# Optimization experiments

Measured on AMD Instinct MI355X. Metric: run time of the kernel, lower is better.

## Reference

```python
import jax, jax.numpy as jnp
import numpy as np
import math

V = 32000; SMAX = 256; N = 512; M = 16; TICKS = 4; D = 512
NSA = 256; NSO = 512; H = 8; HD = D // H; B = 2; S = 256


def _ln(x, g, b, eps=1e-5):
    m = x.mean(-1, keepdims=True)
    v = ((x - m) ** 2).mean(-1, keepdims=True)
    return (x - m) / jnp.sqrt(v + eps) * g + b


def _glu(x):
    a, b = jnp.split(x, 2, axis=-1)
    return a * jax.nn.sigmoid(b)


def setup_inputs() -> dict:
    key = jax.random.key(0)
    ks = iter(jax.random.split(key, 64))
    rn = lambda shape, s: jax.random.normal(next(ks), shape, jnp.float32) * s
    inp = {}
    inp['x'] = jax.random.randint(next(ks), (B, S), 0, V)
    inp['tok_table'] = rn((V, D), 0.02)
    inp['pos_embed'] = rn((SMAX, D), 0.02)
    inp['ln_emb_g'] = jnp.ones(D); inp['ln_emb_b'] = jnp.zeros(D)
    inp['kv_w'] = rn((D, D), 1 / math.sqrt(D)); inp['kv_b'] = jnp.zeros(D)
    inp['kv_ln_g'] = jnp.ones(D); inp['kv_ln_b'] = jnp.zeros(D)
    inp['q_w'] = rn((NSA, D), 1 / math.sqrt(NSA)); inp['q_b'] = jnp.zeros(D)
    inp['wq'] = rn((D, D), 1 / math.sqrt(D)); inp['bq'] = jnp.zeros(D)
    inp['wk'] = rn((D, D), 1 / math.sqrt(D)); inp['bk'] = jnp.zeros(D)
    inp['wv'] = rn((D, D), 1 / math.sqrt(D)); inp['bv'] = jnp.zeros(D)
    inp['ow'] = rn((D, D), 1 / math.sqrt(D)); inp['ob'] = jnp.zeros(D)
    inp['syn_w'] = rn((D + N, 2 * N), 1 / math.sqrt(D + N)); inp['syn_b'] = jnp.zeros(2 * N)
    inp['syn_g'] = jnp.ones(N); inp['syn_beta'] = jnp.zeros(N)
    inp['fc1_w'] = rn((N, M, 256), math.sqrt(2.0 / M)); inp['fc1_b'] = jnp.zeros((N, 256))
    inp['fc2_w'] = rn((N, 128, 2), math.sqrt(2.0 / 128)); inp['fc2_b'] = jnp.zeros((N, 2))
    inp['nlm_T'] = jnp.ones(1)
    a = math.sqrt(1.0 / N)
    inp['start_act'] = jax.random.uniform(next(ks), (SMAX, N), jnp.float32, -a, a)
    b2 = math.sqrt(1.0 / (N + M))
    inp['start_trace'] = jax.random.uniform(next(ks), (SMAX, N, M), jnp.float32, -b2, b2)
    inp['decay_a'] = jnp.zeros(NSA); inp['decay_o'] = jnp.zeros(NSO)
    inp['out_w'] = rn((NSO, V), 1 / math.sqrt(NSO)); inp['out_b'] = jnp.zeros(V)
    inp['idx_al'] = jax.random.randint(next(ks), (NSA,), 0, N)
    inp['idx_ar'] = jax.random.randint(next(ks), (NSA,), 0, N)
    inp['idx_ol'] = jax.random.randint(next(ks), (NSO,), 0, N)
    inp['idx_or'] = jax.random.randint(next(ks), (NSO,), 0, N)
    return inp


def reference(x, tok_table, pos_embed, ln_emb_g, ln_emb_b, kv_w, kv_b, kv_ln_g, kv_ln_b,
              q_w, q_b, wq, bq, wk, bk, wv, bv, ow, ob, syn_w, syn_b, syn_g, syn_beta,
              fc1_w, fc1_b, fc2_w, fc2_b, nlm_T, start_act, start_trace, decay_a, decay_o,
              out_w, out_b, idx_al, idx_ar, idx_ol, idx_or):
    Bz, Sl = x.shape
    emb = _ln(tok_table[x] + pos_embed[:Sl], ln_emb_g, ln_emb_b)        # (B,S,D)
    kv = _ln(emb @ kv_w + kv_b, kv_ln_g, kv_ln_b)
    k = (kv @ wk + bk).reshape(Bz, Sl, H, HD)                            # keys/values fixed over ticks
    v = (kv @ wv + bv).reshape(Bz, Sl, H, HD)
    mask = jnp.triu(jnp.ones((Sl, Sl), bool), 1)                         # True = masked
    r_a = jnp.exp(-decay_a)
    r_o = jnp.exp(-decay_o)
    act = jnp.broadcast_to(start_act[:Sl], (Bz, Sl, N))
    trace = jnp.broadcast_to(start_trace[:Sl], (Bz, Sl, N, M))
    aa = ba = ao_ = bo = None
    preds, certs = [], []
    for _ in range(TICKS):
        # action synchronization (decayed pairwise product)
        pp = act[:, :, idx_al] * act[:, :, idx_ar]
        if aa is None:
            aa, ba = pp, jnp.ones_like(pp)
        else:
            aa, ba = r_a * aa + pp, r_a * ba + 1.0
        sync_a = aa / jnp.sqrt(ba + 1e-8)
        # causal attention with query from action sync
        qh = ((sync_a @ q_w + q_b) @ wq + bq).reshape(Bz, Sl, H, HD)
        sc = jnp.einsum('bqhd,bkhd->bhqk', qh, k) / math.sqrt(HD)
        sc = jnp.where(mask, -1e9, sc)
        attn_out = jnp.einsum('bhqk,bkhd->bqhd', jax.nn.softmax(sc, -1), v).reshape(Bz, Sl, D) @ ow + ob
        # synapse MLP -> new pre-activation, shift memory trace
        state = _ln(_glu(jnp.concatenate([attn_out, act], -1) @ syn_w + syn_b), syn_g, syn_beta)
        trace = jnp.concatenate([trace[..., 1:], state[..., None]], -1)
        # per-neuron NLM (batched private GEMMs)
        h = _glu(jnp.einsum('bsnm,nmh->bsnh', trace, fc1_w) + fc1_b)
        o = _glu(jnp.einsum('bsnh,nho->bsno', h, fc2_w) + fc2_b)
        act = o[..., 0] / nlm_T[0]
        # output synchronization + prediction
        ppo = act[:, :, idx_ol] * act[:, :, idx_or]
        if ao_ is None:
            ao_, bo = ppo, jnp.ones_like(ppo)
        else:
            ao_, bo = r_o * ao_ + ppo, r_o * bo + 1.0
        pred = (ao_ / jnp.sqrt(bo + 1e-8)) @ out_w + out_b                # (B,S,V)
        p = jax.nn.softmax(pred, -1)
        ent = -(p * jnp.log(p + 1e-10)).sum(-1) / math.log(V)
        preds.append(pred)
        certs.append(jnp.stack([ent, 1.0 - ent], -1))
    return jnp.stack(preds, -1), jnp.stack(certs, -1)
```

## Files before the change

### kernel.cpp

```cpp
#include <hip/hip_runtime.h>
#include <cstdint>
#include <cstddef>

#define BATCH 2
#define SEQ   256
#define DIM   512
#define NN    512
#define MM    16
#define NTICK 4
#define NSA   256
#define NSO   512
#define NHEAD 8
#define HDIM  64
#define VOCAB 32000
#define BS    (BATCH*SEQ)

typedef __bf16 bf16;
typedef bf16  bf16x4  __attribute__((ext_vector_type(4)));
typedef bf16  bf16x8v __attribute__((ext_vector_type(8)));
typedef float f32x4   __attribute__((ext_vector_type(4)));

__global__ __launch_bounds__(128) void embed_kernel(const int* __restrict__ x,
    const float* __restrict__ tok, const float* __restrict__ pos, float* __restrict__ out){
  int row = blockIdx.x;
  int s = row & (SEQ-1);
  int token = x[row];
  const float4* tr = (const float4*)(tok + (size_t)token*DIM);
  const float4* pr = (const float4*)(pos + (size_t)s*DIM);
  float4* orow = (float4*)(out + (size_t)row*DIM);
  for (int i = threadIdx.x; i < DIM/4; i += blockDim.x){
    float4 a = tr[i], b = pr[i];
    float4 o; o.x=a.x+b.x; o.y=a.y+b.y; o.z=a.z+b.z; o.w=a.w+b.w;
    orow[i] = o;
  }
}

__global__ __launch_bounds__(256) void ln512_kernel(const float* __restrict__ in,
    const float* __restrict__ g, const float* __restrict__ b, float* __restrict__ out){
  int row = blockIdx.x, tid = threadIdx.x;
  const float* xr = in + (size_t)row*512;
  float v0 = xr[tid], v1 = xr[tid+256];
  float s = v0+v1, ss = v0*v0+v1*v1;
  #pragma unroll
  for (int o = 32; o > 0; o >>= 1){ s += __shfl_down(s, o); ss += __shfl_down(ss, o); }
  __shared__ float rs[4], rss[4];
  __shared__ float smean, sinv;
  int wid = tid >> 6, lane = tid & 63;
  if (lane == 0){ rs[wid] = s; rss[wid] = ss; }
  __syncthreads();
  if (tid == 0){
    float S = rs[0]+rs[1]+rs[2]+rs[3];
    float SS = rss[0]+rss[1]+rss[2]+rss[3];
    float m = S * (1.0f/512.0f);
    float var = SS * (1.0f/512.0f) - m*m;
    smean = m; sinv = 1.0f/sqrtf(var + 1e-5f);
  }
  __syncthreads();
  float m = smean, inv = sinv;
  out[(size_t)row*512 + tid]       = (v0-m)*inv*g[tid]     + b[tid];
  out[(size_t)row*512 + tid + 256] = (v1-m)*inv*g[tid+256] + b[tid+256];
}

__global__ __launch_bounds__(256) void glu_ln_kernel(const float* __restrict__ y,
    const float* __restrict__ g, const float* __restrict__ beta, float* __restrict__ out){
  int row = blockIdx.x, tid = threadIdx.x;
  const float* yr = y + (size_t)row*1024;
  float a0 = yr[tid],     b0 = yr[tid+512];
  float a1 = yr[tid+256], b1 = yr[tid+768];
  float g0 = a0 / (1.0f + expf(-b0));
  float g1 = a1 / (1.0f + expf(-b1));
  float s = g0+g1, ss = g0*g0+g1*g1;
  #pragma unroll
  for (int o = 32; o > 0; o >>= 1){ s += __shfl_down(s, o); ss += __shfl_down(ss, o); }
  __shared__ float rs[4], rss[4];
  __shared__ float smean, sinv;
  int wid = tid >> 6, lane = tid & 63;
  if (lane == 0){ rs[wid] = s; rss[wid] = ss; }
  __syncthreads();
  if (tid == 0){
    float S = rs[0]+rs[1]+rs[2]+rs[3];
    float SS = rss[0]+rss[1]+rss[2]+rss[3];
    float m = S * (1.0f/512.0f);
    float var = SS * (1.0f/512.0f) - m*m;
    smean = m; sinv = 1.0f/sqrtf(var + 1e-5f);
  }
  __syncthreads();
  float m = smean, inv = sinv;
  out[(size_t)row*512 + tid]       = (g0-m)*inv*g[tid]     + beta[tid];
  out[(size_t)row*512 + tid + 256] = (g1-m)*inv*g[tid+256] + beta[tid+256];
}

__global__ __launch_bounds__(256) void sync_kernel(const float* __restrict__ act,
    const int* __restrict__ il, const int* __restrict__ ir, const float* __restrict__ decay,
    float* __restrict__ accA, float* __restrict__ accB,
    float* __restrict__ outf, bf16* __restrict__ outb, int NS, int first){
  int i = blockIdx.x*256 + threadIdx.x;
  if (i >= BS*NS) return;
  int bs = i / NS, c = i - bs*NS;
  const float* ar = act + (size_t)bs*NN;
  float p = ar[il[c]] * ar[ir[c]];
  float A, Bv;
  if (first){ A = p; Bv = 1.0f; }
  else {
    float r = expf(-decay[c]);
    A = r*accA[i] + p;
    Bv = r*accB[i] + 1.0f;
  }
  accA[i] = A; accB[i] = Bv;
  float sy = A / sqrtf(Bv + 1e-8f);
  if (outf) outf[i] = sy;
  if (outb) outb[i] = (bf16)sy;
}

__global__ __launch_bounds__(128) void gemm_f32(
    const float* __restrict__ A, const float* __restrict__ W,
    const float* __restrict__ bias, float* __restrict__ C,
    int Mr, int Nc, int Kd, int lda, int ldc){
  __shared__ float As[16][36];
  __shared__ float Ws[16][64];
  int tid = threadIdx.x;
  int tx = tid & 15, ty = tid >> 4;
  int bm = blockIdx.y * 32, bn = blockIdx.x * 64;
  float acc[4][4] = {};
  int lm = tid >> 2, lkq = tid & 3;
  int wn4 = tid & 15, wkr = tid >> 4;
  for (int k0 = 0; k0 < Kd; k0 += 16){
    float4 a4 = *(const float4*)(A + (size_t)(bm+lm)*lda + k0 + lkq*4);
    float4 w0 = *(const float4*)(W + (size_t)(k0+wkr)*Nc + bn + wn4*4);
    float4 w1 = *(const float4*)(W + (size_t)(k0+wkr+8)*Nc + bn + wn4*4);
    As[lkq*4+0][lm] = a4.x; As[lkq*4+1][lm] = a4.y;
    As[lkq*4+2][lm] = a4.z; As[lkq*4+3][lm] = a4.w;
    *(float4*)&Ws[wkr][wn4*4]   = w0;
    *(float4*)&Ws[wkr+8][wn4*4] = w1;
    __syncthreads();
    #pragma unroll
    for (int kk = 0; kk < 16; kk++){
      float4 av = *(const float4*)&As[kk][ty*4];
      float4 wv = *(const float4*)&Ws[kk][tx*4];
      float ar[4] = {av.x, av.y, av.z, av.w};
      float wr[4] = {wv.x, wv.y, wv.z, wv.w};
      #pragma unroll
      for (int i = 0; i < 4; i++)
        #pragma unroll
        for (int j = 0; j < 4; j++)
          acc[i][j] = fmaf(ar[i], wr[j], acc[i][j]);
    }
    __syncthreads();
  }
  float4 b4 = {0,0,0,0};
  if (bias) b4 = *(const float4*)(bias + bn + tx*4);
  #pragma unroll
  for (int i = 0; i < 4; i++){
    int row = bm + ty*4 + i;
    float4 o;
    o.x = acc[i][0]+b4.x; o.y = acc[i][1]+b4.y;
    o.z = acc[i][2]+b4.z; o.w = acc[i][3]+b4.w;
    *(float4*)(C + (size_t)row*ldc + bn + tx*4) = o;
  }
}

__global__ void qbc_kernel(const float* __restrict__ qb, const float* __restrict__ wq,
                           const float* __restrict__ bq, float* __restrict__ qbc){
  int j = blockIdx.x*64 + threadIdx.x;
  float s = bq[j];
  for (int k = 0; k < DIM; k++) s = fmaf(qb[k], wq[(size_t)k*DIM + j], s);
  qbc[j] = s;
}

__global__ __launch_bounds__(256) void attn_kernel(const float* __restrict__ qh,
    const float* __restrict__ kb, const float* __restrict__ vb, float* __restrict__ outb){
  int qt = blockIdx.x, h = blockIdx.y, b = blockIdx.z;
  __shared__ float qs[16][HDIM];
  __shared__ float sc[16][SEQ + 4];
  __shared__ float red[16][16];
  __shared__ float rowm[16], rowz[16];
  int tid = threadIdx.x;
  {
    int r = tid >> 4, c4 = tid & 15;
    *(float4*)&qs[r][c4*4] =
      *(const float4*)(qh + ((size_t)(b*SEQ + qt*16 + r))*DIM + h*HDIM + c4*4);
  }
  __syncthreads();
  {
    int kk = tid;
    const float* krow = kb + ((size_t)(b*SEQ + kk))*DIM + h*HDIM;
    float s[16] = {};
    for (int d4 = 0; d4 < HDIM/4; d4++){
      float4 k4 = *(const float4*)(krow + d4*4);
      #pragma unroll
      for (int q = 0; q < 16; q++){
        float4 q4 = *(const float4*)&qs[q][d4*4];
        s[q] += q4.x*k4.x + q4.y*k4.y + q4.z*k4.z + q4.w*k4.w;
      }
    }
    #pragma unroll
    for (int q = 0; q < 16; q++){
      int qg = qt*16 + q;
      sc[q][kk] = (kk > qg) ? -1e9f : s[q]*0.125f;
    }
  }
  __syncthreads();
  {
    int q = tid >> 4, seg = tid & 15;
    float m = -1e30f;
    for (int i = 0; i < 16; i++) m = fmaxf(m, sc[q][seg*16+i]);
    red[q][seg] = m;
  }
  __syncthreads();
  if (tid < 16){
    float m = red[tid][0];
    for (int i = 1; i < 16; i++) m = fmaxf(m, red[tid][i]);
    rowm[tid] = m;
  }
  __syncthreads();
  {
    int q = tid >> 4, seg = tid & 15;
    float m = rowm[q], z = 0.0f;
    for (int i = 0; i < 16; i++){
      float e = expf(sc[q][seg*16+i] - m);
      sc[q][seg*16+i] = e;
      z += e;
    }
    red[q][seg] = z;
  }
  __syncthreads();
  if (tid < 16){
    float z = 0.0f;
    for (int i = 0; i < 16; i++) z += red[tid][i];
    rowz[tid] = 1.0f / z;
  }
  __syncthreads();
  {
    int q = tid >> 4, dc = tid & 15;
    float inv = rowz[q];
    float ax=0, ay=0, az=0, aw=0;
    for (int kk = 0; kk < SEQ; kk++){
      float p = sc[q][kk];
      float4 v4 = *(const float4*)(vb + ((size_t)(b*SEQ + kk))*DIM + h*HDIM + dc*4);
      ax = fmaf(p, v4.x, ax); ay = fmaf(p, v4.y, ay);
      az = fmaf(p, v4.z, az); aw = fmaf(p, v4.w, aw);
    }
    float4 o; o.x=ax*inv; o.y=ay*inv; o.z=az*inv; o.w=aw*inv;
    *(float4*)(outb + ((size_t)(b*SEQ + qt*16 + q))*DIM + h*HDIM + dc*4) = o;
  }
}

__global__ void act_init_kernel(const float* __restrict__ sa, float* __restrict__ act){
  int i = blockIdx.x*256 + threadIdx.x;
  act[i] = sa[i & (SEQ*NN - 1)];
}
__global__ void cat_act_kernel(const float* __restrict__ act, float* __restrict__ cat){
  int i = blockIdx.x*256 + threadIdx.x;
  int bs = i >> 9, n = i & 511;
  cat[(size_t)bs*1024 + 512 + n] = act[i];
}

__global__ __launch_bounds__(256) void nlm_kernel(
    const float* __restrict__ start_trace,
    const float* __restrict__ s0, const float* __restrict__ s1,
    const float* __restrict__ s2, const float* __restrict__ s3,
    const float* __restrict__ fc1w, const float* __restrict__ fc1b,
    const float* __restrict__ fc2w, const float* __restrict__ fc2b,
    const float* __restrict__ nlmT, float* __restrict__ act, int t){
  int n = blockIdx.x, b = blockIdx.y, s = threadIdx.x;
  int bs = b*SEQ + s;
  size_t sidx = (size_t)bs*NN + n;
  float tr[16];
  #pragma unroll
  for (int j = 0; j < 16; j++){
    int src = j + t + 1;
    if (src < 16){
      tr[j] = start_trace[((size_t)s*NN + n)*MM + src];
    } else {
      int k = src - 16;
      tr[j] = (k==0) ? s0[sidx] : (k==1) ? s1[sidx] : (k==2) ? s2[sidx] : s3[sidx];
    }
  }
  const float* w1 = fc1w + (size_t)n*16*256;
  const float* b1 = fc1b + (size_t)n*256;
  const float* w2 = fc2w + (size_t)n*256;
  float o0 = fc2b[n*2+0], o1 = fc2b[n*2+1];
  #pragma unroll 4
  for (int j = 0; j < 128; j++){
    float a  = b1[j];
    float bb = b1[j+128];
    #pragma unroll
    for (int m = 0; m < 16; m++){
      a  = fmaf(tr[m], w1[m*256 + j],       a);
      bb = fmaf(tr[m], w1[m*256 + j + 128], bb);
    }
    float gg = a / (1.0f + expf(-bb));
    o0 = fmaf(gg, w2[j*2+0], o0);
    o1 = fmaf(gg, w2[j*2+1], o1);
  }
  float o = o0 / (1.0f + expf(-o1));
  act[sidx] = o / nlmT[0];
}

__global__ __launch_bounds__(256) void out_gemm(
    const bf16* __restrict__ sy0, const bf16* __restrict__ sy1,
    const bf16* __restrict__ sy2, const bf16* __restrict__ sy3,
    const float* __restrict__ Wo, const float* __restrict__ bo,
    float* __restrict__ outp){
  __shared__ bf16 BsT[128][40];
  int tid = threadIdx.x;
  int m0 = blockIdx.x * 64;
  int n0 = blockIdx.y * 128;
  int wid = tid >> 6, lane = tid & 63;
  int ln = lane & 15, kq = lane >> 4;
  int mrow = m0 + wid*16 + ln;
  const bf16* sy[4] = {sy0, sy1, sy2, sy3};
  f32x4 acc[4][8];
  #pragma unroll
  for (int t = 0; t < 4; t++)
    #pragma unroll
    for (int nt = 0; nt < 8; nt++) acc[t][nt] = (f32x4){0.f,0.f,0.f,0.f};
  int snq = tid & 31, sk2 = tid >> 5;
  for (int k0 = 0; k0 < 512; k0 += 32){
    {
      const float* src = Wo + (size_t)(k0 + sk2*4)*VOCAB + n0 + snq*4;
      float4 r0 = *(const float4*)(src);
      float4 r1 = *(const float4*)(src + VOCAB);
      float4 r2 = *(const float4*)(src + 2*(size_t)VOCAB);
      float4 r3 = *(const float4*)(src + 3*(size_t)VOCAB);
      float c0[4] = {r0.x,r0.y,r0.z,r0.w};
      float c1[4] = {r1.x,r1.y,r1.z,r1.w};
      float c2[4] = {r2.x,r2.y,r2.z,r2.w};
      float c3[4] = {r3.x,r3.y,r3.z,r3.w};
      #pragma unroll
      for (int i = 0; i < 4; i++){
        bf16x4 pk;
        pk[0]=(bf16)c0[i]; pk[1]=(bf16)c1[i]; pk[2]=(bf16)c2[i]; pk[3]=(bf16)c3[i];
        *(bf16x4*)&BsT[snq*4+i][sk2*4] = pk;
      }
    }
    __syncthreads();
    bf16x8v af[4];
    #pragma unroll
    for (int t = 0; t < 4; t++)
      af[t] = *(const bf16x8v*)(sy[t] + (size_t)mrow*512 + k0 + kq*8);
    #pragma unroll
    for (int nt = 0; nt < 8; nt++){
      bf16x8v bfr = *(const bf16x8v*)&BsT[nt*16 + ln][kq*8];
      #pragma unroll
      for (int t = 0; t < 4; t++)
        acc[t][nt] = __builtin_amdgcn_mfma_f32_16x16x32_bf16(af[t], bfr, acc[t][nt], 0, 0, 0);
    }
    __syncthreads();
  }
  #pragma unroll
  for (int nt = 0; nt < 8; nt++){
    int col = n0 + nt*16 + ln;
    float bb = bo[col];
    #pragma unroll
    for (int r = 0; r < 4; r++){
      int row = m0 + wid*16 + kq*4 + r;
      float4 o;
      o.x = acc[0][nt][r] + bb;
      o.y = acc[1][nt][r] + bb;
      o.z = acc[2][nt][r] + bb;
      o.w = acc[3][nt][r] + bb;
      *(float4*)(outp + ((size_t)row*VOCAB + col)*4) = o;
    }
  }
}

__global__ __launch_bounds__(256) void entropy_kernel(
    const float* __restrict__ preds, float* __restrict__ certs){
  int bs = blockIdx.x, tid = threadIdx.x;
  const float4* row = (const float4*)(preds + (size_t)bs*VOCAB*4);
  float m0=-1e30f, m1=-1e30f, m2=-1e30f, m3=-1e30f;
  for (int v = tid; v < VOCAB; v += 256){
    float4 x = row[v];
    m0 = fmaxf(m0, x.x); m1 = fmaxf(m1, x.y);
    m2 = fmaxf(m2, x.z); m3 = fmaxf(m3, x.w);
  }
  #pragma unroll
  for (int o = 32; o > 0; o >>= 1){
    m0 = fmaxf(m0, __shfl_down(m0, o)); m1 = fmaxf(m1, __shfl_down(m1, o));
    m2 = fmaxf(m2, __shfl_down(m2, o)); m3 = fmaxf(m3, __shfl_down(m3, o));
  }
  __shared__ float rm[4][4];
  __shared__ float fm[4];
  int wid = tid >> 6, lane = tid & 63;
  if (lane == 0){ rm[wid][0]=m0; rm[wid][1]=m1; rm[wid][2]=m2; rm[wid][3]=m3; }
  __syncthreads();
  if (tid == 0){
    #pragma unroll
    for (int t = 0; t < 4; t++)
      fm[t] = fmaxf(fmaxf(rm[0][t], rm[1][t]), fmaxf(rm[2][t], rm[3][t]));
  }
  __syncthreads();
  m0=fm[0]; m1=fm[1]; m2=fm[2]; m3=fm[3];
  float z0=0,z1=0,z2=0,z3=0, s0=0,s1=0,s2=0,s3=0;
  for (int v = tid; v < VOCAB; v += 256){
    float4 x = row[v];
    float e;
    e = expf(x.x-m0); z0 += e; s0 = fmaf(e, x.x-m0, s0);
    e = expf(x.y-m1); z1 += e; s1 = fmaf(e, x.y-m1, s1);
    e = expf(x.z-m2); z2 += e; s2 = fmaf(e, x.z-m2, s2);
    e = expf(x.w-m3); z3 += e; s3 = fmaf(e, x.w-m3, s3);
  }
  #pragma unroll
  for (int o = 32; o > 0; o >>= 1){
    z0 += __shfl_down(z0,o); z1 += __shfl_down(z1,o);
    z2 += __shfl_down(z2,o); z3 += __shfl_down(z3,o);
    s0 += __shfl_down(s0,o); s1 += __shfl_down(s1,o);
    s2 += __shfl_down(s2,o); s3 += __shfl_down(s3,o);
  }
  __shared__ float rz[4][8];
  if (lane == 0){
    rz[wid][0]=z0; rz[wid][1]=z1; rz[wid][2]=z2; rz[wid][3]=z3;
    rz[wid][4]=s0; rz[wid][5]=s1; rz[wid][6]=s2; rz[wid][7]=s3;
  }
  __syncthreads();
  if (tid == 0){
    float inv_logV = 1.0f / logf((float)VOCAB);
    #pragma unroll
    for (int t = 0; t < 4; t++){
      float Z = rz[0][t]+rz[1][t]+rz[2][t]+rz[3][t];
      float Ss = rz[0][t+4]+rz[1][t+4]+rz[2][t+4]+rz[3][t+4];
      float ent = (logf(Z) - Ss/Z) * inv_logV;
      certs[((size_t)bs*2 + 0)*4 + t] = ent;
      certs[((size_t)bs*2 + 1)*4 + t] = 1.0f - ent;
    }
  }
}

extern "C" void kernel_launch(void* const* d_in, const int* in_sizes, int n_in,
                              void* d_out, int out_size, void* d_ws, size_t ws_size,
                              hipStream_t stream){
  const int*   x        = (const int*)  d_in[0];
  const float* tok      = (const float*)d_in[1];
  const float* pos      = (const float*)d_in[2];
  const float* ln_emb_g = (const float*)d_in[3];
  const float* ln_emb_b = (const float*)d_in[4];
  const float* kv_w     = (const float*)d_in[5];
  const float* kv_b     = (const float*)d_in[6];
  const float* kv_ln_g  = (const float*)d_in[7];
  const float* kv_ln_b  = (const float*)d_in[8];
  const float* q_w      = (const float*)d_in[9];
  const float* q_b      = (const float*)d_in[10];
  const float* wq       = (const float*)d_in[11];
  const float* bq       = (const float*)d_in[12];
  const float* wk       = (const float*)d_in[13];
  const float* bk       = (const float*)d_in[14];
  const float* wv       = (const float*)d_in[15];
  const float* bv       = (const float*)d_in[16];
  const float* ow       = (const float*)d_in[17];
  const float* ob       = (const float*)d_in[18];
  const float* syn_w    = (const float*)d_in[19];
  const float* syn_b    = (const float*)d_in[20];
  const float* syn_g    = (const float*)d_in[21];
  const float* syn_beta = (const float*)d_in[22];
  const float* fc1_w    = (const float*)d_in[23];
  const float* fc1_b    = (const float*)d_in[24];
  const float* fc2_w    = (const float*)d_in[25];
  const float* fc2_b    = (const float*)d_in[26];
  const float* nlm_T    = (const float*)d_in[27];
  const float* start_act   = (const float*)d_in[28];
  const float* start_trace = (const float*)d_in[29];
  const float* decay_a  = (const float*)d_in[30];
  const float* decay_o  = (const float*)d_in[31];
  const float* out_w    = (const float*)d_in[32];
  const float* out_b    = (const float*)d_in[33];
  const int* idx_al = (const int*)d_in[34];
  const int* idx_ar = (const int*)d_in[35];
  const int* idx_ol = (const int*)d_in[36];
  const int* idx_or = (const int*)d_in[37];

  char* wp = (char*)d_ws;
  auto alloc = [&](size_t bytes) -> void* {
    void* p = (void*)wp;
    wp += (bytes + 255) & ~(size_t)255;
    return p;
  };
  float* qwc      = (float*)alloc((size_t)256*512*4);
  float* qbc      = (float*)alloc(512*4);
  float* emb_raw  = (float*)alloc((size_t)BS*512*4);
  float* emb      = (float*)alloc((size_t)BS*512*4);
  float* kvt      = (float*)alloc((size_t)BS*512*4);
  float* kvn      = (float*)alloc((size_t)BS*512*4);
  float* kbuf     = (float*)alloc((size_t)BS*512*4);
  float* vbuf     = (float*)alloc((size_t)BS*512*4);
  float* act      = (float*)alloc((size_t)BS*512*4);
  float* aaB      = (float*)alloc((size_t)BS*256*4);
  float* baB      = (float*)alloc((size_t)BS*256*4);
  float* aoB      = (float*)alloc((size_t)BS*512*4);
  float* boB      = (float*)alloc((size_t)BS*512*4);
  float* sync_a   = (float*)alloc((size_t)BS*256*4);
  float* qh       = (float*)alloc((size_t)BS*512*4);
  float* attn_raw = (float*)alloc((size_t)BS*512*4);
  float* catb     = (float*)alloc((size_t)BS*1024*4);
  float* syn_y    = (float*)alloc((size_t)BS*1024*4);
  float* states[NTICK];
  for (int t = 0; t < NTICK; t++) states[t] = (float*)alloc((size_t)BS*512*4);
  bf16* syob[NTICK];
  for (int t = 0; t < NTICK; t++) syob[t] = (bf16*)alloc((size_t)BS*512*2);

  float* preds = (float*)d_out;
  float* certs = (float*)d_out + (size_t)BS*VOCAB*NTICK;

  embed_kernel<<<BS, 128, 0, stream>>>(x, tok, pos, emb_raw);
  ln512_kernel<<<BS, 256, 0, stream>>>(emb_raw, ln_emb_g, ln_emb_b, emb);
  gemm_f32<<<dim3(512/64, 512/32), 128, 0, stream>>>(emb, kv_w, kv_b, kvt, 512,512,512, 512,512);
  ln512_kernel<<<BS, 256, 0, stream>>>(kvt, kv_ln_g, kv_ln_b, kvn);
  gemm_f32<<<dim3(512/64, 512/32), 128, 0, stream>>>(kvn, wk, bk, kbuf, 512,512,512, 512,512);
  gemm_f32<<<dim3(512/64, 512/32), 128, 0, stream>>>(kvn, wv, bv, vbuf, 512,512,512, 512,512);
  gemm_f32<<<dim3(512/64, 256/32), 128, 0, stream>>>(q_w, wq, nullptr, qwc, 256,512,512, 512,512);
  qbc_kernel<<<8, 64, 0, stream>>>(q_b, wq, bq, qbc);
  act_init_kernel<<<(BS*NN)/256, 256, 0, stream>>>(start_act, act);

  for (int t = 0; t < NTICK; t++){
    sync_kernel<<<(BS*NSA)/256, 256, 0, stream>>>(act, idx_al, idx_ar, decay_a,
        aaB, baB, sync_a, nullptr, NSA, t==0);
    gemm_f32<<<dim3(512/64, 512/32), 128, 0, stream>>>(sync_a, qwc, qbc, qh, 512,512,256, 256,512);
    attn_kernel<<<dim3(16, NHEAD, BATCH), 256, 0, stream>>>(qh, kbuf, vbuf, attn_raw);
    gemm_f32<<<dim3(512/64, 512/32), 128, 0, stream>>>(attn_raw, ow, ob, catb, 512,512,512, 512,1024);
    cat_act_kernel<<<(BS*NN)/256, 256, 0, stream>>>(act, catb);
    gemm_f32<<<dim3(1024/64, 512/32), 128, 0, stream>>>(catb, syn_w, syn_b, syn_y, 512,1024,1024, 1024,1024);
    glu_ln_kernel<<<BS, 256, 0, stream>>>(syn_y, syn_g, syn_beta, states[t]);
    nlm_kernel<<<dim3(NN, BATCH), 256, 0, stream>>>(start_trace,
        states[0], states[1], states[2], states[3],
        fc1_w, fc1_b, fc2_w, fc2_b, nlm_T, act, t);
    sync_kernel<<<(BS*NSO)/256, 256, 0, stream>>>(act, idx_ol, idx_or, decay_o,
        aoB, boB, nullptr, syob[t], NSO, t==0);
  }

  out_gemm<<<dim3(BS/64, VOCAB/128), 256, 0, stream>>>(
      syob[0], syob[1], syob[2], syob[3], out_w, out_b, preds);
  entropy_kernel<<<BS, 256, 0, stream>>>(preds, certs);
}
```

Before: 1.643 ms.

## Use split-bf16 MFMA GEMMs, pre-transposed bf16 weights, and fuse entropy into output GEMM

Replaces the scalar fp32 GEMM with an MFMA kernel that emulates fp32 precision using three bf16 products (hi*hi, lo*hi, hi*lo) on pre-split, transposed weights. The output projection now reads a pre-transposed bf16 copy of out_w directly, without staging through shared memory. It also computes per-block softmax max, sum and entropy partials in its epilogue, and a small kernel merges them, so the separate full pass over the logits is gone. In exchange, extra weight split/transpose kernels run on every call, and precision drops slightly.

```diff
diff --git a/kernel.cpp b/kernel.cpp
--- a/kernel.cpp
+++ b/kernel.cpp
@@ -14,6 +14,7 @@
 #define HDIM  64
 #define VOCAB 32000
 #define BS    (BATCH*SEQ)
+#define NBLK  250
 
 typedef __bf16 bf16;
 typedef bf16  bf16x4  __attribute__((ext_vector_type(4)));
@@ -112,50 +113,68 @@
   if (outb) outb[i] = (bf16)sy;
 }
 
-__global__ __launch_bounds__(128) void gemm_f32(
-    const float* __restrict__ A, const float* __restrict__ W,
-    const float* __restrict__ bias, float* __restrict__ C,
-    int Mr, int Nc, int Kd, int lda, int ldc){
-  __shared__ float As[16][36];
-  __shared__ float Ws[16][64];
+__global__ __launch_bounds__(256) void split_t(const float* __restrict__ W,
+    bf16* __restrict__ hiT, bf16* __restrict__ loT, int K, int N){
+  __shared__ float t[32][33];
+  int n0 = blockIdx.x*32, k0 = blockIdx.y*32;
   int tid = threadIdx.x;
-  int tx = tid & 15, ty = tid >> 4;
-  int bm = blockIdx.y * 32, bn = blockIdx.x * 64;
-  float acc[4][4] = {};
-  int lm = tid >> 2, lkq = tid & 3;
-  int wn4 = tid & 15, wkr = tid >> 4;
-  for (int k0 = 0; k0 < Kd; k0 += 16){
-    float4 a4 = *(const float4*)(A + (size_t)(bm+lm)*lda + k0 + lkq*4);
-    float4 w0 = *(const float4*)(W + (size_t)(k0+wkr)*Nc + bn + wn4*4);
-    float4 w1 = *(const float4*)(W + (size_t)(k0+wkr+8)*Nc + bn + wn4*4);
-    As[lkq*4+0][lm] = a4.x; As[lkq*4+1][lm] = a4.y;
-    As[lkq*4+2][lm] = a4.z; As[lkq*4+3][lm] = a4.w;
-    *(float4*)&Ws[wkr][wn4*4]   = w0;
-    *(float4*)&Ws[wkr+8][wn4*4] = w1;
-    __syncthreads();
-    #pragma unroll
-    for (int kk = 0; kk < 16; kk++){
-      float4 av = *(const float4*)&As[kk][ty*4];
-      float4 wv = *(const float4*)&Ws[kk][tx*4];
-      float ar[4] = {av.x, av.y, av.z, av.w};
-      float wr[4] = {wv.x, wv.y, wv.z, wv.w};
-      #pragma unroll
-      for (int i = 0; i < 4; i++)
-        #pragma unroll
-        for (int j = 0; j < 4; j++)
-          acc[i][j] = fmaf(ar[i], wr[j], acc[i][j]);
-    }
-    __syncthreads();
-  }
-  float4 b4 = {0,0,0,0};
-  if (bias) b4 = *(const float4*)(bias + bn + tx*4);
-  #pragma unroll
-  for (int i = 0; i < 4; i++){
-    int row = bm + ty*4 + i;
-    float4 o;
-    o.x = acc[i][0]+b4.x; o.y = acc[i][1]+b4.y;
-    o.z = acc[i][2]+b4.z; o.w = acc[i][3]+b4.w;
-    *(float4*)(C + (size_t)row*ldc + bn + tx*4) = o;
+  int r = tid >> 3, c4 = (tid & 7)*4;
+  float4 v = *(const float4*)(W + (size_t)(k0+r)*N + n0 + c4);
+  t[r][c4+0]=v.x; t[r][c4+1]=v.y; t[r][c4+2]=v.z; t[r][c4+3]=v.w;
+  __syncthreads();
+  bf16x4 hi, lo;
+  #pragma unroll
+  for (int j = 0; j < 4; j++){
+    float a = t[c4+j][r];
+    bf16 h = (bf16)a;
+    hi[j] = h;
+    lo[j] = (bf16)(a - (float)h);
+  }
+  *(bf16x4*)(hiT + (size_t)(n0+r)*K + k0 + c4) = hi;
+  if (loT) *(bf16x4*)(loT + (size_t)(n0+r)*K + k0 + c4) = lo;
+}
+
+__global__ __launch_bounds__(64) void gemm_x3(
+    const float* __restrict__ A, const bf16* __restrict__ WhT,
+    const bf16* __restrict__ WlT, const float* __restrict__ bias,
+    float* __restrict__ C, int K, int lda, int ldc){
+  int n0 = blockIdx.x * 64, m0 = blockIdx.y * 16;
+  int lane = threadIdx.x;
+  int ln = lane & 15, kq = lane >> 4;
+  f32x4 acc[4];
+  #pragma unroll
+  for (int nf = 0; nf < 4; nf++) acc[nf] = (f32x4){0.f,0.f,0.f,0.f};
+  const float* arow = A + (size_t)(m0 + ln)*lda + kq*8;
+  const bf16* w0h = WhT + (size_t)(n0 + ln)*K + kq*8;
+  const bf16* w0l = WlT + (size_t)(n0 + ln)*K + kq*8;
+  size_t nstep = (size_t)16*K;
+  for (int k0 = 0; k0 < K; k0 += 32){
+    float4 a0 = *(const float4*)(arow + k0);
+    float4 a1 = *(const float4*)(arow + k0 + 4);
+    float av[8] = {a0.x,a0.y,a0.z,a0.w,a1.x,a1.y,a1.z,a1.w};
+    bf16x8v ahi, alo;
+    #pragma unroll
+    for (int j = 0; j < 8; j++){
+      bf16 h = (bf16)av[j];
+      ahi[j] = h;
+      alo[j] = (bf16)(av[j] - (float)h);
+    }
+    #pragma unroll
+    for (int nf = 0; nf < 4; nf++){
+      bf16x8v bh = *(const bf16x8v*)(w0h + nf*nstep + k0);
+      bf16x8v bl = *(const bf16x8v*)(w0l + nf*nstep + k0);
+      acc[nf] = __builtin_amdgcn_mfma_f32_16x16x32_bf16(ahi, bh, acc[nf], 0,0,0);
+      acc[nf] = __builtin_amdgcn_mfma_f32_16x16x32_bf16(alo, bh, acc[nf], 0,0,0);
+      acc[nf] = __builtin_amdgcn_mfma_f32_16x16x32_bf16(ahi, bl, acc[nf], 0,0,0);
+    }
+  }
+  #pragma unroll
+  for (int nf = 0; nf < 4; nf++){
+    int col = n0 + nf*16 + ln;
+    float bb = bias ? bias[col] : 0.0f;
+    #pragma unroll
+    for (int r = 0; r < 4; r++)
+      C[(size_t)(m0 + kq*4 + r)*ldc + col] = acc[nf][r] + bb;
   }
 }
 
@@ -297,133 +316,149 @@
   act[sidx] = o / nlmT[0];
 }
 
-__global__ __launch_bounds__(256) void out_gemm(
+__global__ __launch_bounds__(256) void out_gemm2(
     const bf16* __restrict__ sy0, const bf16* __restrict__ sy1,
     const bf16* __restrict__ sy2, const bf16* __restrict__ sy3,
-    const float* __restrict__ Wo, const float* __restrict__ bo,
-    float* __restrict__ outp){
-  __shared__ bf16 BsT[128][40];
+    const bf16* __restrict__ WoT, const float* __restrict__ bo,
+    float* __restrict__ outp, float* __restrict__ pm,
+    float* __restrict__ pz, float* __restrict__ ps){
+  int m0 = blockIdx.x * 16;
+  int n0 = blockIdx.y * 128;
   int tid = threadIdx.x;
-  int m0 = blockIdx.x * 64;
-  int n0 = blockIdx.y * 128;
-  int wid = tid >> 6, lane = tid & 63;
+  int w = tid >> 6, lane = tid & 63;
   int ln = lane & 15, kq = lane >> 4;
-  int mrow = m0 + wid*16 + ln;
-  const bf16* sy[4] = {sy0, sy1, sy2, sy3};
-  f32x4 acc[4][8];
+  int nb = n0 + w*32;
+  f32x4 acc[4][2];
+  #pragma unroll
+  for (int t = 0; t < 4; t++){
+    acc[t][0] = (f32x4){0.f,0.f,0.f,0.f};
+    acc[t][1] = (f32x4){0.f,0.f,0.f,0.f};
+  }
+  size_t aoff = (size_t)(m0 + ln)*512 + kq*8;
+  const bf16* a0p = sy0 + aoff;
+  const bf16* a1p = sy1 + aoff;
+  const bf16* a2p = sy2 + aoff;
+  const bf16* a3p = sy3 + aoff;
+  const bf16* b0p = WoT + (size_t)(nb + ln)*512 + kq*8;
+  const bf16* b1p = b0p + (size_t)16*512;
+  for (int k0 = 0; k0 < 512; k0 += 32){
+    bf16x8v av0 = *(const bf16x8v*)(a0p + k0);
+    bf16x8v av1 = *(const bf16x8v*)(a1p + k0);
+    bf16x8v av2 = *(const bf16x8v*)(a2p + k0);
+    bf16x8v av3 = *(const bf16x8v*)(a3p + k0);
+    bf16x8v bv0 = *(const bf16x8v*)(b0p + k0);
+    bf16x8v bv1 = *(const bf16x8v*)(b1p + k0);
+    acc[0][0] = __builtin_amdgcn_mfma_f32_16x16x32_bf16(av0, bv0, acc[0][0], 0,0,0);
+    acc[1][0] = __builtin_amdgcn_mfma_f32_16x16x32_bf16(av1, bv0, acc[1][0], 0,0,0);
+    acc[2][0] = __builtin_amdgcn_mfma_f32_16x16x32_bf16(av2, bv0, acc[2][0], 0,0,0);
+    acc[3][0] = __builtin_amdgcn_mfma_f32_16x16x32_bf16(av3, bv0, acc[3][0], 0,0,0);
+    acc[0][1] = __builtin_amdgcn_mfma_f32_16x16x32_bf16(av0, bv1, acc[0][1], 0,0,0);
+    acc[1][1] = __builtin_amdgcn_mfma_f32_16x16x32_bf16(av1, bv1, acc[1][1], 0,0,0);
+    acc[2][1] = __builtin_amdgcn_mfma_f32_16x16x32_bf16(av2, bv1, acc[2][1], 0,0,0);
+    acc[3][1] = __builtin_amdgcn_mfma_f32_16x16x32_bf16(av3, bv1, acc[3][1], 0,0,0);
+  }
+  float bb0 = bo[nb + ln], bb1 = bo[nb + 16 + ln];
   #pragma unroll
   for (int t = 0; t < 4; t++)
     #pragma unroll
-    for (int nt = 0; nt < 8; nt++) acc[t][nt] = (f32x4){0.f,0.f,0.f,0.f};
-  int snq = tid & 31, sk2 = tid >> 5;
-  for (int k0 = 0; k0 < 512; k0 += 32){
-    {
-      const float* src = Wo + (size_t)(k0 + sk2*4)*VOCAB + n0 + snq*4;
-      float4 r0 = *(const float4*)(src);
-      float4 r1 = *(const float4*)(src + VOCAB);
-      float4 r2 = *(const float4*)(src + 2*(size_t)VOCAB);
-      float4 r3 = *(const float4*)(src + 3*(size_t)VOCAB);
-      float c0[4] = {r0.x,r0.y,r0.z,r0.w};
-      float c1[4] = {r1.x,r1.y,r1.z,r1.w};
-      float c2[4] = {r2.x,r2.y,r2.z,r2.w};
-      float c3[4] = {r3.x,r3.y,r3.z,r3.w};
+    for (int r = 0; r < 4; r++){ acc[t][0][r] += bb0; acc[t][1][r] += bb1; }
+  #pragma unroll
+  for (int r = 0; r < 4; r++){
+    size_t rowoff = (size_t)(m0 + kq*4 + r)*VOCAB;
+    float4 o0, o1;
+    o0.x=acc[0][0][r]; o0.y=acc[1][0][r]; o0.z=acc[2][0][r]; o0.w=acc[3][0][r];
+    o1.x=acc[0][1][r]; o1.y=acc[1][1][r]; o1.z=acc[2][1][r]; o1.w=acc[3][1][r];
+    *(float4*)(outp + (rowoff + nb + ln)*4)      = o0;
+    *(float4*)(outp + (rowoff + nb + 16 + ln)*4) = o1;
+  }
+  __shared__ float redm[4][4][16], redz[4][4][16], reds[4][4][16];
+  float gm[4][4];
+  #pragma unroll
+  for (int t = 0; t < 4; t++)
+    #pragma unroll
+    for (int r = 0; r < 4; r++){
+      float m = fmaxf(acc[t][0][r], acc[t][1][r]);
       #pragma unroll
-      for (int i = 0; i < 4; i++){
-        bf16x4 pk;
-        pk[0]=(bf16)c0[i]; pk[1]=(bf16)c1[i]; pk[2]=(bf16)c2[i]; pk[3]=(bf16)c3[i];
-        *(bf16x4*)&BsT[snq*4+i][sk2*4] = pk;
+      for (int o2 = 1; o2 < 16; o2 <<= 1) m = fmaxf(m, __shfl_xor(m, o2));
+      gm[t][r] = m;
+    }
+  if (ln == 0){
+    #pragma unroll
+    for (int t = 0; t < 4; t++)
+      #pragma unroll
+      for (int r = 0; r < 4; r++) redm[w][t][kq*4+r] = gm[t][r];
+  }
+  __syncthreads();
+  #pragma unroll
+  for (int t = 0; t < 4; t++)
+    #pragma unroll
+    for (int r = 0; r < 4; r++){
+      int row = kq*4+r;
+      gm[t][r] = fmaxf(fmaxf(redm[0][t][row], redm[1][t][row]),
+                       fmaxf(redm[2][t][row], redm[3][t][row]));
+    }
+  float zz[4][4], ssv[4][4];
+  #pragma unroll
+  for (int t = 0; t < 4; t++)
+    #pragma unroll
+    for (int r = 0; r < 4; r++){
+      float v0 = acc[t][0][r] - gm[t][r];
+      float v1 = acc[t][1][r] - gm[t][r];
+      float e0 = expf(v0), e1 = expf(v1);
+      float z = e0 + e1;
+      float s = v0*e0 + v1*e1;
+      #pragma unroll
+      for (int o2 = 1; o2 < 16; o2 <<= 1){ z += __shfl_xor(z, o2); s += __shfl_xor(s, o2); }
+      zz[t][r] = z; ssv[t][r] = s;
+    }
+  if (ln == 0){
+    #pragma unroll
+    for (int t = 0; t < 4; t++)
+      #pragma unroll
+      for (int r = 0; r < 4; r++){ redz[w][t][kq*4+r] = zz[t][r]; reds[w][t][kq*4+r] = ssv[t][r]; }
+  }
+  __syncthreads();
+  if (w == 0 && ln == 0){
+    #pragma unroll
+    for (int t = 0; t < 4; t++)
+      #pragma unroll
+      for (int r = 0; r < 4; r++){
+        int row = kq*4 + r;
+        float Z = redz[0][t][row]+redz[1][t][row]+redz[2][t][row]+redz[3][t][row];
+        float S = reds[0][t][row]+reds[1][t][row]+reds[2][t][row]+reds[3][t][row];
+        size_t p = ((size_t)(m0+row)*4 + t)*NBLK + blockIdx.y;
+        pm[p] = gm[t][r]; pz[p] = Z; ps[p] = S;
       }
-    }
-    __syncthreads();
-    bf16x8v af[4];
-    #pragma unroll
-    for (int t = 0; t < 4; t++)
-      af[t] = *(const bf16x8v*)(sy[t] + (size_t)mrow*512 + k0 + kq*8);
-    #pragma unroll
-    for (int nt = 0; nt < 8; nt++){
-      bf16x8v bfr = *(const bf16x8v*)&BsT[nt*16 + ln][kq*8];
-      #pragma unroll
-      for (int t = 0; t < 4; t++)
-        acc[t][nt] = __builtin_amdgcn_mfma_f32_16x16x32_bf16(af[t], bfr, acc[t][nt], 0, 0, 0);
-    }
-    __syncthreads();
-  }
-  #pragma unroll
-  for (int nt = 0; nt < 8; nt++){
-    int col = n0 + nt*16 + ln;
-    float bb = bo[col];
-    #pragma unroll
-    for (int r = 0; r < 4; r++){
-      int row = m0 + wid*16 + kq*4 + r;
-      float4 o;
-      o.x = acc[0][nt][r] + bb;
-      o.y = acc[1][nt][r] + bb;
-      o.z = acc[2][nt][r] + bb;
-      o.w = acc[3][nt][r] + bb;
-      *(float4*)(outp + ((size_t)row*VOCAB + col)*4) = o;
-    }
-  }
-}
-
-__global__ __launch_bounds__(256) void entropy_kernel(
-    const float* __restrict__ preds, float* __restrict__ certs){
-  int bs = blockIdx.x, tid = threadIdx.x;
-  const float4* row = (const float4*)(preds + (size_t)bs*VOCAB*4);
-  float m0=-1e30f, m1=-1e30f, m2=-1e30f, m3=-1e30f;
-  for (int v = tid; v < VOCAB; v += 256){
-    float4 x = row[v];
-    m0 = fmaxf(m0, x.x); m1 = fmaxf(m1, x.y);
-    m2 = fmaxf(m2, x.z); m3 = fmaxf(m3, x.w);
-  }
-  #pragma unroll
-  for (int o = 32; o > 0; o >>= 1){
-    m0 = fmaxf(m0, __shfl_down(m0, o)); m1 = fmaxf(m1, __shfl_down(m1, o));
-    m2 = fmaxf(m2, __shfl_down(m2, o)); m3 = fmaxf(m3, __shfl_down(m3, o));
-  }
-  __shared__ float rm[4][4];
-  __shared__ float fm[4];
-  int wid = tid >> 6, lane = tid & 63;
-  if (lane == 0){ rm[wid][0]=m0; rm[wid][1]=m1; rm[wid][2]=m2; rm[wid][3]=m3; }
-  __syncthreads();
-  if (tid == 0){
-    #pragma unroll
-    for (int t = 0; t < 4; t++)
-      fm[t] = fmaxf(fmaxf(rm[0][t], rm[1][t]), fmaxf(rm[2][t], rm[3][t]));
-  }
-  __syncthreads();
-  m0=fm[0]; m1=fm[1]; m2=fm[2]; m3=fm[3];
-  float z0=0,z1=0,z2=0,z3=0, s0=0,s1=0,s2=0,s3=0;
-  for (int v = tid; v < VOCAB; v += 256){
-    float4 x = row[v];
-    float e;
-    e = expf(x.x-m0); z0 += e; s0 = fmaf(e, x.x-m0, s0);
-    e = expf(x.y-m1); z1 += e; s1 = fmaf(e, x.y-m1, s1);
-    e = expf(x.z-m2); z2 += e; s2 = fmaf(e, x.z-m2, s2);
-    e = expf(x.w-m3); z3 += e; s3 = fmaf(e, x.w-m3, s3);
-  }
-  #pragma unroll
-  for (int o = 32; o > 0; o >>= 1){
-    z0 += __shfl_down(z0,o); z1 += __shfl_down(z1,o);
-    z2 += __shfl_down(z2,o); z3 += __shfl_down(z3,o);
-    s0 += __shfl_down(s0,o); s1 += __shfl_down(s1,o);
-    s2 += __shfl_down(s2,o); s3 += __shfl_down(s3,o);
-  }
-  __shared__ float rz[4][8];
+  }
+}
+
+__global__ __launch_bounds__(64) void ent_final(const float* __restrict__ pm,
+    const float* __restrict__ pz, const float* __restrict__ ps, float* __restrict__ certs){
+  int row = blockIdx.x >> 2, t = blockIdx.x & 3;
+  const size_t base = ((size_t)row*4 + t)*NBLK;
+  int lane = threadIdx.x;
+  float M = -1e30f, Z = 0.0f, S = 0.0f;
+  for (int i = lane; i < NBLK; i += 64){
+    float m2 = pm[base+i], z2 = pz[base+i], s2 = ps[base+i];
+    float Mn = fmaxf(M, m2);
+    float e1 = expf(M - Mn), e2 = expf(m2 - Mn);
+    S = (S + (M - Mn)*Z)*e1 + (s2 + (m2 - Mn)*z2)*e2;
+    Z = Z*e1 + z2*e2;
+    M = Mn;
+  }
+  #pragma unroll
+  for (int o = 1; o < 64; o <<= 1){
+    float m2 = __shfl_xor(M, o), z2 = __shfl_xor(Z, o), s2 = __shfl_xor(S, o);
+    float Mn = fmaxf(M, m2);
+    float e1 = expf(M - Mn), e2 = expf(m2 - Mn);
+    S = (S + (M - Mn)*Z)*e1 + (s2 + (m2 - Mn)*z2)*e2;
+    Z = Z*e1 + z2*e2;
+    M = Mn;
+  }
   if (lane == 0){
-    rz[wid][0]=z0; rz[wid][1]=z1; rz[wid][2]=z2; rz[wid][3]=z3;
-    rz[wid][4]=s0; rz[wid][5]=s1; rz[wid][6]=s2; rz[wid][7]=s3;
-  }
-  __syncthreads();
-  if (tid == 0){
-    float inv_logV = 1.0f / logf((float)VOCAB);
-    #pragma unroll
-    for (int t = 0; t < 4; t++){
-      float Z = rz[0][t]+rz[1][t]+rz[2][t]+rz[3][t];
-      float Ss = rz[0][t+4]+rz[1][t+4]+rz[2][t+4]+rz[3][t+4];
-      float ent = (logf(Z) - Ss/Z) * inv_logV;
-      certs[((size_t)bs*2 + 0)*4 + t] = ent;
-      certs[((size_t)bs*2 + 1)*4 + t] = 1.0f - ent;
-    }
+    float ent = (logf(Z) - S/Z) * (1.0f / logf((float)VOCAB));
+    certs[((size_t)row*2 + 0)*4 + t] = ent;
+    certs[((size_t)row*2 + 1)*4 + t] = 1.0f - ent;
   }
 }
 
@@ -497,28 +532,55 @@
   for (int t = 0; t < NTICK; t++) states[t] = (float*)alloc((size_t)BS*512*4);
   bf16* syob[NTICK];
   for (int t = 0; t < NTICK; t++) syob[t] = (bf16*)alloc((size_t)BS*512*2);
+  bf16* kvT_h = (bf16*)alloc((size_t)512*512*2);
+  bf16* kvT_l = (bf16*)alloc((size_t)512*512*2);
+  bf16* wkT_h = (bf16*)alloc((size_t)512*512*2);
+  bf16* wkT_l = (bf16*)alloc((size_t)512*512*2);
+  bf16* wvT_h = (bf16*)alloc((size_t)512*512*2);
+  bf16* wvT_l = (bf16*)alloc((size_t)512*512*2);
+  bf16* owT_h = (bf16*)alloc((size_t)512*512*2);
+  bf16* owT_l = (bf16*)alloc((size_t)512*512*2);
+  bf16* wqT_h = (bf16*)alloc((size_t)512*512*2);
+  bf16* wqT_l = (bf16*)alloc((size_t)512*512*2);
+  bf16* synT_h = (bf16*)alloc((size_t)1024*1024*2);
+  bf16* synT_l = (bf16*)alloc((size_t)1024*1024*2);
+  bf16* qwcT_h = (bf16*)alloc((size_t)512*256*2);
+  bf16* qwcT_l = (bf16*)alloc((size_t)512*256*2);
+  bf16* WoT    = (bf16*)alloc((size_t)VOCAB*512*2);
+  float* pm = (float*)alloc((size_t)BS*4*NBLK*4);
+  float* pz = (float*)alloc((size_t)BS*4*NBLK*4);
+  float* ps = (float*)alloc((size_t)BS*4*NBLK*4);
 
   float* preds = (float*)d_out;
   float* certs = (float*)d_out + (size_t)BS*VOCAB*NTICK;
 
+  split_t<<<dim3(16,16), 256, 0, stream>>>(kv_w,  kvT_h, kvT_l, 512, 512);
+  split_t<<<dim3(16,16), 256, 0, stream>>>(wk,    wkT_h, wkT_l, 512, 512);
+  split_t<<<dim3(16,16), 256, 0, stream>>>(wv,    wvT_h, wvT_l, 512, 512);
+  split_t<<<dim3(16,16), 256, 0, stream>>>(ow,    owT_h, owT_l, 512, 512);
+  split_t<<<dim3(16,16), 256, 0, stream>>>(wq,    wqT_h, wqT_l, 512, 512);
+  split_t<<<dim3(32,32), 256, 0, stream>>>(syn_w, synT_h, synT_l, 1024, 1024);
+  split_t<<<dim3(VOCAB/32,16), 256, 0, stream>>>(out_w, WoT, nullptr, 512, VOCAB);
+
   embed_kernel<<<BS, 128, 0, stream>>>(x, tok, pos, emb_raw);
   ln512_kernel<<<BS, 256, 0, stream>>>(emb_raw, ln_emb_g, ln_emb_b, emb);
-  gemm_f32<<<dim3(512/64, 512/32), 128, 0, stream>>>(emb, kv_w, kv_b, kvt, 512,512,512, 512,512);
+  gemm_x3<<<dim3(8,32), 64, 0, stream>>>(emb, kvT_h, kvT_l, kv_b, kvt, 512, 512, 512);
   ln512_kernel<<<BS, 256, 0, stream>>>(kvt, kv_ln_g, kv_ln_b, kvn);
-  gemm_f32<<<dim3(512/64, 512/32), 128, 0, stream>>>(kvn, wk, bk, kbuf, 512,512,512, 512,512);
-  gemm_f32<<<dim3(512/64, 512/32), 128, 0, stream>>>(kvn, wv, bv, vbuf, 512,512,512, 512,512);
-  gemm_f32<<<dim3(512/64, 256/32), 128, 0, stream>>>(q_w, wq, nullptr, qwc, 256,512,512, 512,512);
+  gemm_x3<<<dim3(8,32), 64, 0, stream>>>(kvn, wkT_h, wkT_l, bk, kbuf, 512, 512, 512);
+  gemm_x3<<<dim3(8,32), 64, 0, stream>>>(kvn, wvT_h, wvT_l, bv, vbuf, 512, 512, 512);
+  gemm_x3<<<dim3(8,16), 64, 0, stream>>>(q_w, wqT_h, wqT_l, nullptr, qwc, 512, 512, 512);
+  split_t<<<dim3(16,8), 256, 0, stream>>>(qwc, qwcT_h, qwcT_l, 256, 512);
   qbc_kernel<<<8, 64, 0, stream>>>(q_b, wq, bq, qbc);
   act_init_kernel<<<(BS*NN)/256, 256, 0, stream>>>(start_act, act);
 
   for (int t = 0; t < NTICK; t++){
     sync_kernel<<<(BS*NSA)/256, 256, 0, stream>>>(act, idx_al, idx_ar, decay_a,
         aaB, baB, sync_a, nullptr, NSA, t==0);
-    gemm_f32<<<dim3(512/64, 512/32), 128, 0, stream>>>(sync_a, qwc, qbc, qh, 512,512,256, 256,512);
+    gemm_x3<<<dim3(8,32), 64, 0, stream>>>(sync_a, qwcT_h, qwcT_l, qbc, qh, 256, 256, 512);
     attn_kernel<<<dim3(16, NHEAD, BATCH), 256, 0, stream>>>(qh, kbuf, vbuf, attn_raw);
-    gemm_f32<<<dim3(512/64, 512/32), 128, 0, stream>>>(attn_raw, ow, ob, catb, 512,512,512, 512,1024);
+    gemm_x3<<<dim3(8,32), 64, 0, stream>>>(attn_raw, owT_h, owT_l, ob, catb, 512, 512, 1024);
     cat_act_kernel<<<(BS*NN)/256, 256, 0, stream>>>(act, catb);
-    gemm_f32<<<dim3(1024/64, 512/32), 128, 0, stream>>>(catb, syn_w, syn_b, syn_y, 512,1024,1024, 1024,1024);
+    gemm_x3<<<dim3(16,32), 64, 0, stream>>>(catb, synT_h, synT_l, syn_b, syn_y, 1024, 1024, 1024);
     glu_ln_kernel<<<BS, 256, 0, stream>>>(syn_y, syn_g, syn_beta, states[t]);
     nlm_kernel<<<dim3(NN, BATCH), 256, 0, stream>>>(start_trace,
         states[0], states[1], states[2], states[3],
@@ -527,7 +589,7 @@
         aoB, boB, nullptr, syob[t], NSO, t==0);
   }
 
-  out_gemm<<<dim3(BS/64, VOCAB/128), 256, 0, stream>>>(
-      syob[0], syob[1], syob[2], syob[3], out_w, out_b, preds);
-  entropy_kernel<<<BS, 256, 0, stream>>>(preds, certs);
-}
+  out_gemm2<<<dim3(32, NBLK), 256, 0, stream>>>(
+      syob[0], syob[1], syob[2], syob[3], WoT, out_b, preds, pm, pz, ps);
+  ent_final<<<BS*4, 64, 0, stream>>>(pm, pz, ps, certs);
+}
```

Result: faster. 1.564 ms (-4.8%).
